# Performance work log

Measured on AMD Instinct MI355X. Metric: run time of the kernel, lower is better.

Reference implementation:

```python
import jax, jax.numpy as jnp
import numpy as np

STEPS = 32
LO, HI = 0.0, 1.0
BETA = 0.1
IMPULSE = float(1.0 / (abs(BETA) * np.sqrt(np.pi)))  # unused in fwd, kept for parity


def _cells(x):
    """Filtration values of all cells of the V-construction cubical complex.
    Vertices = pixels; edges = max of the 2 endpoint pixels; squares = max of 4 corners."""
    v = x                                                    # [B,C,H,W]   sign +1
    he = jnp.maximum(x[..., :, :-1], x[..., :, 1:])          # [B,C,H,W-1] sign -1
    ve = jnp.maximum(x[..., :-1, :], x[..., 1:, :])          # [B,C,H-1,W] sign -1
    sq = jnp.maximum(jnp.maximum(x[..., :-1, :-1], x[..., :-1, 1:]),
                     jnp.maximum(x[..., 1:, :-1], x[..., 1:, 1:]))  # [B,C,H-1,W-1] sign +1
    return v, he, ve, sq


def _ecc_forward(x):
    """Euler characteristic curve ECC(t) = #V(t) - #E(t) + #F(t) sampled on
    tseq = linspace(LO, HI, STEPS). Returns [B, C*STEPS] (flattened, matching nn.Flatten)."""
    B, C, H, W = x.shape
    BC = B * C
    tseq = jnp.linspace(LO, HI, STEPS, dtype=x.dtype)
    v, he, ve, sq = _cells(x)
    f = jnp.concatenate([v.reshape(BC, -1), he.reshape(BC, -1),
                         ve.reshape(BC, -1), sq.reshape(BC, -1)], axis=1)  # [BC, Ncells]
    signs = jnp.concatenate([
        jnp.ones(H * W, jnp.float32),
        -jnp.ones(H * (W - 1), jnp.float32),
        -jnp.ones((H - 1) * W, jnp.float32),
        jnp.ones((H - 1) * (W - 1), jnp.float32),
    ])
    # first threshold index j with tseq[j] >= f (cell is "alive" for all t >= idx)
    idx = jnp.searchsorted(tseq, f, side='left')            # [BC, Ncells], values in [0, STEPS]
    rows = jnp.arange(BC)[:, None]
    hist = jnp.zeros((BC, STEPS + 1), jnp.float32).at[rows, idx].add(signs[None, :])
    ecc = jnp.cumsum(hist[:, :STEPS], axis=1)               # [BC, STEPS]
    return ecc.reshape(B, C * STEPS)


def setup_inputs() -> dict:
    key = jax.random.key(0)
    x = jax.random.uniform(key, (64, 3, 224, 224), dtype=jnp.float32)
    return {"x": x}


def reference(x):
    return _ecc_forward(x)
```

## Files before the change

kernel.cpp:

```cpp
#include <hip/hip_runtime.h>
#include <hip/hip_bf16.h>


#define H 224
#define W 224
#define STEPS 32
#define NBINS 33
#define NCOL 64
#define BANDS 8
#define BAND_ROWS 28
#define SUB_ROWS 7
#define NTHR 256

__device__ __forceinline__ int bin_of(float f) {
    return (int)ceilf(f * 31.0f);
}

__global__ __launch_bounds__(NTHR, 6) void ecc_hist_kernel(
        const float* __restrict__ x, int* __restrict__ part)
{
    __shared__ int lh[NBINS * NCOL];

    const int tid = threadIdx.x;
    for (int i = tid; i < NBINS * NCOL; i += NTHR) lh[i] = 0;
    __syncthreads();

    const int band = blockIdx.x & (BANDS - 1);
    const int img  = blockIdx.x / BANDS;
    const float* __restrict__ p = x + (size_t)img * (H * W);

    const int c = tid & 63;
    const int s = tid >> 6;

    if (c < 56) {
        const int  j0     = c << 2;
        const bool lastc  = (c == 55);
        const bool firstc = (c == 0);
        const int  jn = lastc  ? (j0 + 3) : (j0 + 4);
        const int  jp = firstc ? j0       : (j0 - 1);
        const int  r0 = band * BAND_ROWS + s * SUB_ROWS;
        int* __restrict__ lhc = lh + c;

        const float* __restrict__ row0 = p + r0 * W;
        float4 F = *(const float4*)(row0 + j0);
        int B0 = bin_of(F.x), B1 = bin_of(F.y), B2 = bin_of(F.z), B3 = bin_of(F.w);
        int Bn = lastc  ? 0  : bin_of(row0[jn]);
        int Bp = firstc ? 63 : bin_of(row0[jp]);

        for (int k = 0; k < SUB_ROWS; ++k) {
            const int r = r0 + k;

            {
                int dm = (B0 > Bp) ? 1 : 0;
                int d0 = (B1 > B0) ? 1 : 0;
                int d1 = (B2 > B1) ? 1 : 0;
                int d2 = (B3 > B2) ? 1 : 0;
                int d3 = (Bn > B3) ? 1 : 0;
                int v0 = d0 - dm, v1 = d1 - d0, v2 = d2 - d1, v3 = d3 - d2;
                if (v0) atomicAdd(&lhc[B0 << 6], v0);
                if (v1) atomicAdd(&lhc[B1 << 6], v1);
                if (v2) atomicAdd(&lhc[B2 << 6], v2);
                if (v3) atomicAdd(&lhc[B3 << 6], v3);
            }

            if (r < H - 1) {
                const float* __restrict__ row1 = p + (r + 1) * W;
                float4 G = *(const float4*)(row1 + j0);
                int C0 = bin_of(G.x), C1 = bin_of(G.y),
                    C2 = bin_of(G.z), C3 = bin_of(G.w);
                int Cn = lastc  ? 0  : bin_of(row1[jn]);
                int Cp = firstc ? 63 : bin_of(row1[jp]);

                int M0 = max(B0, C0), M1 = max(B1, C1),
                    M2 = max(B2, C2), M3 = max(B3, C3);
                int Mn = max(Bn, Cn), Mp = max(Bp, Cp);
                int em = (M0 > Mp) ? 1 : 0;
                int e0 = (M1 > M0) ? 1 : 0;
                int e1 = (M2 > M1) ? 1 : 0;
                int e2 = (M3 > M2) ? 1 : 0;
                int e3 = (Mn > M3) ? 1 : 0;
                int w0 = em - e0, w1 = e0 - e1, w2 = e1 - e2, w3 = e2 - e3;
                if (w0) atomicAdd(&lhc[M0 << 6], w0);
                if (w1) atomicAdd(&lhc[M1 << 6], w1);
                if (w2) atomicAdd(&lhc[M2 << 6], w2);
                if (w3) atomicAdd(&lhc[M3 << 6], w3);

                B0 = C0; B1 = C1; B2 = C2; B3 = C3; Bn = Cn; Bp = Cp;
            }
        }
    }
    __syncthreads();

    const int b = tid >> 3;
    const int g = tid & 7;
    const int4* rowp = (const int4*)(lh + (b << 6) + (g << 3));
    int4 u0 = rowp[0], u1 = rowp[1];
    int sum = u0.x + u0.y + u0.z + u0.w + u1.x + u1.y + u1.z + u1.w;
    sum += __shfl_xor(sum, 1);
    sum += __shfl_xor(sum, 2);
    sum += __shfl_xor(sum, 4);
    if (g == 0)
        part[(((img << 3) | band) << 5) + b] = sum;
}

__global__ __launch_bounds__(64) void ecc_cumsum_kernel(
        const int* __restrict__ part, float* __restrict__ out)
{
    const int img  = blockIdx.x;
    const int lane = threadIdx.x;
    if (lane < STEPS) {
        const int* pb = part + (img << 8) + lane;
        int s = 0;
        #pragma unroll
        for (int band = 0; band < BANDS; ++band) s += pb[band << 5];
        #pragma unroll
        for (int off = 1; off < STEPS; off <<= 1) {
            int v = __shfl_up(s, off);
            if (lane >= off) s += v;
        }
        out[img * STEPS + lane] = (float)s;
    }
}

extern "C" void kernel_launch(void* const* d_in, const int* in_sizes, int n_in,
                              void* d_out, int out_size, void* d_ws, size_t ws_size,
                              hipStream_t stream) {
    const float* x = (const float*)d_in[0];
    float* out = (float*)d_out;
    int* part = (int*)d_ws;

    const int nimg = in_sizes[0] / (H * W);

    dim3 grid1(nimg * BANDS);
    ecc_hist_kernel<<<grid1, NTHR, 0, stream>>>(x, part);

    ecc_cumsum_kernel<<<dim3(nimg), 64, 0, stream>>>(part, out);
}
```

Measured before the change: 79.41 us.

## Share neighbor bins via wavefront shuffles and drop atomic predicates

Neighbouring-column bin values now come from cross-lane shuffles instead of extra scalar global loads per row. The ceil-based binning becomes a single fmaf plus truncation. The conditional atomics are made unconditional to avoid divergent branches. The trade-off is more LDS atomic traffic, including adds of zero, and a binning formula that may differ from ceil at exact boundaries. Lanes 56-63 sit idle inside the branch, so shuffle correctness depends on lanes 0-55 sharing a wavefront.

Result: faster. 76.83 us (-3.3%).

```diff
diff --git a/kernel.cpp b/kernel.cpp
--- a/kernel.cpp
+++ b/kernel.cpp
@@ -13,7 +13,7 @@
 #define NTHR 256
 
 __device__ __forceinline__ int bin_of(float f) {
-    return (int)ceilf(f * 31.0f);
+    return (int)fmaf(f, 31.0f, 0.99999994f);
 }
 
 __global__ __launch_bounds__(NTHR, 6) void ecc_hist_kernel(
@@ -33,43 +33,37 @@
     const int s = tid >> 6;
 
     if (c < 56) {
-        const int  j0     = c << 2;
         const bool lastc  = (c == 55);
         const bool firstc = (c == 0);
-        const int  jn = lastc  ? (j0 + 3) : (j0 + 4);
-        const int  jp = firstc ? j0       : (j0 - 1);
         const int  r0 = band * BAND_ROWS + s * SUB_ROWS;
         int* __restrict__ lhc = lh + c;
 
-        const float* __restrict__ row0 = p + r0 * W;
-        float4 F = *(const float4*)(row0 + j0);
+        const float* __restrict__ row = p + r0 * W + (c << 2);
+        float4 F = *(const float4*)row;
         int B0 = bin_of(F.x), B1 = bin_of(F.y), B2 = bin_of(F.z), B3 = bin_of(F.w);
-        int Bn = lastc  ? 0  : bin_of(row0[jn]);
-        int Bp = firstc ? 63 : bin_of(row0[jp]);
+        int t;
+        t = __shfl_down(B0, 1); int Bn = lastc  ? 64 : t;
+        t = __shfl_up  (B3, 1); int Bp = firstc ? 63 : t;
 
         for (int k = 0; k < SUB_ROWS; ++k) {
-            const int r = r0 + k;
-
             {
                 int dm = (B0 > Bp) ? 1 : 0;
                 int d0 = (B1 > B0) ? 1 : 0;
                 int d1 = (B2 > B1) ? 1 : 0;
                 int d2 = (B3 > B2) ? 1 : 0;
                 int d3 = (Bn > B3) ? 1 : 0;
-                int v0 = d0 - dm, v1 = d1 - d0, v2 = d2 - d1, v3 = d3 - d2;
-                if (v0) atomicAdd(&lhc[B0 << 6], v0);
-                if (v1) atomicAdd(&lhc[B1 << 6], v1);
-                if (v2) atomicAdd(&lhc[B2 << 6], v2);
-                if (v3) atomicAdd(&lhc[B3 << 6], v3);
+                atomicAdd(&lhc[B0 << 6], d0 - dm);
+                atomicAdd(&lhc[B1 << 6], d1 - d0);
+                atomicAdd(&lhc[B2 << 6], d2 - d1);
+                atomicAdd(&lhc[B3 << 6], d3 - d2);
             }
 
-            if (r < H - 1) {
-                const float* __restrict__ row1 = p + (r + 1) * W;
-                float4 G = *(const float4*)(row1 + j0);
+            if (r0 + k < H - 1) {
+                float4 G = *(const float4*)(row + W);
                 int C0 = bin_of(G.x), C1 = bin_of(G.y),
                     C2 = bin_of(G.z), C3 = bin_of(G.w);
-                int Cn = lastc  ? 0  : bin_of(row1[jn]);
-                int Cp = firstc ? 63 : bin_of(row1[jp]);
+                t = __shfl_down(C0, 1); int Cn = lastc  ? 64 : t;
+                t = __shfl_up  (C3, 1); int Cp = firstc ? 63 : t;
 
                 int M0 = max(B0, C0), M1 = max(B1, C1),
                     M2 = max(B2, C2), M3 = max(B3, C3);
@@ -79,14 +73,14 @@
                 int e1 = (M2 > M1) ? 1 : 0;
                 int e2 = (M3 > M2) ? 1 : 0;
                 int e3 = (Mn > M3) ? 1 : 0;
-                int w0 = em - e0, w1 = e0 - e1, w2 = e1 - e2, w3 = e2 - e3;
-                if (w0) atomicAdd(&lhc[M0 << 6], w0);
-                if (w1) atomicAdd(&lhc[M1 << 6], w1);
-                if (w2) atomicAdd(&lhc[M2 << 6], w2);
-                if (w3) atomicAdd(&lhc[M3 << 6], w3);
+                atomicAdd(&lhc[M0 << 6], em - e0);
+                atomicAdd(&lhc[M1 << 6], e0 - e1);
+                atomicAdd(&lhc[M2 << 6], e1 - e2);
+                atomicAdd(&lhc[M3 << 6], e2 - e3);
 
                 B0 = C0; B1 = C1; B2 = C2; B3 = C3; Bn = Cn; Bp = Cp;
             }
+            row += W;
         }
     }
     __syncthreads();
```
